# Kernel tuning notes

Hardware: AMD Instinct MI355X
Metric: run time of the kernel (lower is better)

The kernel has to match this reference:

```python
import jax, jax.numpy as jnp
import numpy as np

EMBED = 1024
HEADS = 16
DK = EMBED // HEADS
DFF = 4 * EMBED
EPS = 1e-5


def layer_norm(x, g, b):
    mu = jnp.mean(x, axis=-1, keepdims=True)
    var = jnp.var(x, axis=-1, keepdims=True)
    return (x - mu) * jax.lax.rsqrt(var + EPS) * g + b


def setup_inputs() -> dict:
    key = jax.random.key(0)
    ks = jax.random.split(key, 12)
    s = lambda d: 1.0 / np.sqrt(d)
    return {
        "x": jax.random.normal(ks[0], (4, 1024, EMBED), dtype=jnp.float32),
        "norm_g": jnp.ones((EMBED,), jnp.float32),
        "norm_b": jnp.zeros((EMBED,), jnp.float32),
        "w_qkv": jax.random.normal(ks[1], (EMBED, 3 * EMBED), jnp.float32) * s(EMBED),
        "b_qkv": jnp.zeros((3 * EMBED,), jnp.float32),
        "w_proj": jax.random.normal(ks[2], (EMBED, EMBED), jnp.float32) * s(EMBED),
        "b_proj": jnp.zeros((EMBED,), jnp.float32),
        "w_fc1": jax.random.normal(ks[3], (EMBED, DFF), jnp.float32) * s(EMBED),
        "b_fc1": jnp.zeros((DFF,), jnp.float32),
        "w_fc2": jax.random.normal(ks[4], (DFF, EMBED), jnp.float32) * s(DFF),
        "b_fc2": jnp.zeros((EMBED,), jnp.float32),
    }


def reference(x, norm_g, norm_b, w_qkv, b_qkv, w_proj, b_proj, w_fc1, b_fc1, w_fc2, b_fc2):
    B, N, C = x.shape
    # --- attention branch (pre-norm, shared norm params) ---
    h = layer_norm(x, norm_g, norm_b)
    qkv = (h @ w_qkv + b_qkv).reshape(B, N, 3, HEADS, DK)
    q, k, v = jnp.moveaxis(qkv, 2, 0)  # each [B, N, H, dk]
    # NOTE: source divides by dk**(-0.5), i.e. multiplies scores by sqrt(dk)
    scores = jnp.einsum('bnhd,bmhd->bhnm', q, k) * (DK ** 0.5)
    attn = jax.nn.softmax(scores, axis=-1)
    ctx = jnp.einsum('bhnm,bmhd->bnhd', attn, v).reshape(B, N, C)
    x = x + (ctx @ w_proj + b_proj)
    # --- MLP branch ---
    h = layer_norm(x, norm_g, norm_b)
    h = jax.nn.gelu(h @ w_fc1 + b_fc1, approximate=False)
    x = x + (h @ w_fc2 + b_fc2)
    return x
```

## Files before the change

### kernel.cpp

```cpp
#include <hip/hip_runtime.h>
#include <hip/hip_bf16.h>

typedef __attribute__((ext_vector_type(8))) short short8;
typedef __attribute__((ext_vector_type(8))) _Float16 half8;
typedef __attribute__((ext_vector_type(4))) float f32x4;

__device__ __forceinline__ unsigned short f2h(float f) {
    _Float16 h = (_Float16)f;
    return *reinterpret_cast<unsigned short*>(&h);
}
__device__ __forceinline__ float h2f(unsigned short u) {
    _Float16 h = *reinterpret_cast<_Float16*>(&u);
    return (float)h;
}

__device__ __forceinline__ void gld_lds16(const unsigned short* g, unsigned short* l) {
    __builtin_amdgcn_global_load_lds(
        (const __attribute__((address_space(1))) unsigned int*)g,
        (__attribute__((address_space(3))) unsigned int*)l, 16, 0, 0);
}

__global__ __launch_bounds__(256)
void transpose_all(const float* __restrict__ W0, const float* __restrict__ W1,
                   const float* __restrict__ W2, const float* __restrict__ W3,
                   unsigned short* __restrict__ o0, unsigned short* __restrict__ o1,
                   unsigned short* __restrict__ o2, unsigned short* __restrict__ o3) {
    __shared__ float tile[32][33];
    const int bid = blockIdx.x;
    const float* W; unsigned short* out; int K, N, loc;
    if (bid < 3072)      { W = W0; out = o0; K = 1024; N = 3072; loc = bid; }
    else if (bid < 4096) { W = W1; out = o1; K = 1024; N = 1024; loc = bid - 3072; }
    else if (bid < 8192) { W = W2; out = o2; K = 1024; N = 4096; loc = bid - 4096; }
    else                 { W = W3; out = o3; K = 4096; N = 1024; loc = bid - 8192; }
    const int nx = N >> 5;
    const int n0 = (loc % nx) << 5, k0 = (loc / nx) << 5;
    const int tid = threadIdx.x;
    const int r = tid >> 3, c4 = (tid & 7) << 2;
    float4 v = *reinterpret_cast<const float4*>(W + (size_t)(k0 + r) * N + n0 + c4);
    tile[r][c4 + 0] = v.x; tile[r][c4 + 1] = v.y;
    tile[r][c4 + 2] = v.z; tile[r][c4 + 3] = v.w;
    __syncthreads();
    const int n = n0 + r;
    ushort4 o;
    o.x = f2h(tile[c4 + 0][r]); o.y = f2h(tile[c4 + 1][r]);
    o.z = f2h(tile[c4 + 2][r]); o.w = f2h(tile[c4 + 3][r]);
    *reinterpret_cast<ushort4*>(out + (size_t)n * K + k0 + c4) = o;
}

__global__ __launch_bounds__(256)
void ln_kernel(const float* __restrict__ x, const float* __restrict__ gw,
               const float* __restrict__ bw, unsigned short* __restrict__ out) {
    const int row = blockIdx.x, tid = threadIdx.x;
    const float* xr = x + (size_t)row * 1024;
    float4 v = *reinterpret_cast<const float4*>(xr + tid * 4);
    float s = v.x + v.y + v.z + v.w;
    float sq = v.x * v.x + v.y * v.y + v.z * v.z + v.w * v.w;
    #pragma unroll
    for (int off = 1; off < 64; off <<= 1) {
        s  += __shfl_xor(s, off);
        sq += __shfl_xor(sq, off);
    }
    __shared__ float ps[4], pq[4];
    const int wave = tid >> 6;
    if ((tid & 63) == 0) { ps[wave] = s; pq[wave] = sq; }
    __syncthreads();
    s  = ps[0] + ps[1] + ps[2] + ps[3];
    sq = pq[0] + pq[1] + pq[2] + pq[3];
    const float mu = s * (1.0f / 1024.0f);
    const float var = sq * (1.0f / 1024.0f) - mu * mu;
    const float rs = rsqrtf(var + 1e-5f);
    float4 gv = *reinterpret_cast<const float4*>(gw + tid * 4);
    float4 bv = *reinterpret_cast<const float4*>(bw + tid * 4);
    ushort4 o;
    o.x = f2h((v.x - mu) * rs * gv.x + bv.x);
    o.y = f2h((v.y - mu) * rs * gv.y + bv.y);
    o.z = f2h((v.z - mu) * rs * gv.z + bv.z);
    o.w = f2h((v.w - mu) * rs * gv.w + bv.w);
    *reinterpret_cast<ushort4*>(out + (size_t)row * 1024 + tid * 4) = o;
}

template<int EPI>
__global__ __launch_bounds__(512, 2)
void gemm256(const unsigned short* __restrict__ A, const unsigned short* __restrict__ Bt,
             const float* __restrict__ bias, void* Cout,
             int M, int N, int K, int lda, int ldb, int ldc) {
    __shared__ unsigned short As[2][256 * 64];
    __shared__ unsigned short Bs[2][256 * 64];
    const int tid = threadIdx.x;
    const int wave = tid >> 6, lane = tid & 63;
    const int nwg = gridDim.x;
    const int swz = (blockIdx.x & 7) * (nwg >> 3) + (blockIdx.x >> 3);
    const int nx = N >> 8;
    const int bm = (swz / nx) << 8, bn = (swz % nx) << 8;
    const int wm = wave >> 2, wn = wave & 3;
    const int fr = lane & 15, g8 = (lane >> 4) << 3, fq = (lane >> 4) << 2;
    const int jq = g8 >> 3;
    const int sx = fr & 7;

    const int srow = lane >> 3;
    const int scol = ((lane & 7) ^ srow) << 3;
    const unsigned short* gA = A + (size_t)(bm + wave * 32 + srow) * lda + scol;
    const unsigned short* gB = Bt + (size_t)(bn + wave * 32 + srow) * ldb + scol;
    const int lb = wave * 32 * 64;

    f32x4 acc[8][4];
    #pragma unroll
    for (int m = 0; m < 8; ++m)
        #pragma unroll
        for (int n_ = 0; n_ < 4; ++n_)
            #pragma unroll
            for (int r_ = 0; r_ < 4; ++r_) acc[m][n_][r_] = 0.0f;

    auto stage = [&](int buf, int k0) {
        #pragma unroll
        for (int i = 0; i < 4; ++i) {
            gld_lds16(gA + (size_t)(i * 8) * lda + k0, &As[buf][lb + i * 512]);
            gld_lds16(gB + (size_t)(i * 8) * ldb + k0, &Bs[buf][lb + i * 512]);
        }
    };
    auto compute = [&](int buf) {
        half8 bf0[4], bf1[4];
        #pragma unroll
        for (int n_ = 0; n_ < 4; ++n_) {
            const int bb = (wn * 64 + n_ * 16 + fr) * 64;
            bf0[n_] = *reinterpret_cast<const half8*>(&Bs[buf][bb + ((jq ^ sx) << 3)]);
            bf1[n_] = *reinterpret_cast<const half8*>(&Bs[buf][bb + (((4 + jq) ^ sx) << 3)]);
        }
        #pragma unroll
        for (int m = 0; m < 8; ++m) {
            const int ab = (wm * 128 + m * 16 + fr) * 64;
            half8 a0 = *reinterpret_cast<const half8*>(&As[buf][ab + ((jq ^ sx) << 3)]);
            half8 a1 = *reinterpret_cast<const half8*>(&As[buf][ab + (((4 + jq) ^ sx) << 3)]);
            #pragma unroll
            for (int n_ = 0; n_ < 4; ++n_) {
                acc[m][n_] = __builtin_amdgcn_mfma_f32_16x16x32_f16(a0, bf0[n_], acc[m][n_], 0, 0, 0);
                acc[m][n_] = __builtin_amdgcn_mfma_f32_16x16x32_f16(a1, bf1[n_], acc[m][n_], 0, 0, 0);
            }
        }
    };

    stage(0, 0);
    __syncthreads();
    const int NT = K >> 6;
    for (int t = 0; t < NT; ++t) {
        const int cur = t & 1;
        if (t + 1 < NT) stage(cur ^ 1, (t + 1) << 6);
        compute(cur);
        __syncthreads();
    }

    unsigned short* o16 = reinterpret_cast<unsigned short*>(Cout);
    #pragma unroll
    for (int n_ = 0; n_ < 4; ++n_) {
        const int col = bn + wn * 64 + n_ * 16 + fr;
        const float bc = bias[col];
        #pragma unroll
        for (int m = 0; m < 8; ++m) {
            #pragma unroll
            for (int r_ = 0; r_ < 4; ++r_) {
                const int row = bm + wm * 128 + m * 16 + fq + r_;
                const size_t idx = (size_t)row * ldc + col;
                float v = acc[m][n_][r_] + bc;
                if (EPI == 0) {
                    o16[idx] = f2h(v);
                } else {
                    float ge = 0.5f * v * (1.0f + erff(v * 0.70710678118654752f));
                    o16[idx] = f2h(ge);
                }
            }
        }
    }
}

template<int EPI, int BM>
__global__ __launch_bounds__(256)
void gemm_bt(const unsigned short* __restrict__ A, const unsigned short* __restrict__ Bt,
             const float* __restrict__ bias, const float* resid,
             void* Cout, int M, int N, int K, int lda, int ldb, int ldc) {
    constexpr int MF = BM / 32;
    __shared__ unsigned short As[2][BM * 32];
    __shared__ unsigned short Bs[2][128 * 32];
    const int tid = threadIdx.x;
    const int wave = tid >> 6, lane = tid & 63;
    const int bm = blockIdx.y * BM, bn = blockIdx.x << 7;
    const int wr = (wave >> 1) * (BM / 2), wc = (wave & 1) << 6;
    const int fr = lane & 15, g8 = (lane >> 4) << 3, fq = (lane >> 4) << 2;
    const int jq = g8 >> 3, sx2 = (fr >> 1) & 3;
    const size_t koff = (EPI == 3) ? (size_t)blockIdx.z * K : 0;

    const int srowA = (BM == 128) ? ((wave << 5) + (lane >> 2)) : ((wave << 4) + (lane >> 2));
    const int srowB = (wave << 5) + (lane >> 2);
    const int scol = (((lane & 3) ^ ((lane >> 3) & 3))) << 3;
    const unsigned short* gA0 = A + (size_t)(bm + srowA) * lda + scol + koff;
    const unsigned short* gA1 = gA0 + (size_t)16 * lda;
    const unsigned short* gB0 = Bt + (size_t)(bn + srowB) * ldb + scol + koff;
    const unsigned short* gB1 = gB0 + (size_t)16 * ldb;

    f32x4 acc[MF][4];
    #pragma unroll
    for (int m = 0; m < MF; ++m)
        #pragma unroll
        for (int n = 0; n < 4; ++n)
            #pragma unroll
            for (int r = 0; r < 4; ++r) acc[m][n][r] = 0.0f;

    auto stage = [&](int buf, int k0) {
        unsigned short* lA = &As[buf][(BM == 128) ? (wave << 10) : (wave << 9)];
        unsigned short* lB = &Bs[buf][wave << 10];
        gld_lds16(gA0 + k0, lA);
        if constexpr (BM == 128) gld_lds16(gA1 + k0, lA + 512);
        gld_lds16(gB0 + k0, lB);
        gld_lds16(gB1 + k0, lB + 512);
    };
    auto compute = [&](int buf) {
        half8 af[MF], bfv[4];
        #pragma unroll
        for (int m = 0; m < MF; ++m)
            af[m] = *reinterpret_cast<const half8*>(
                &As[buf][(wr + m * 16 + fr) * 32 + ((jq ^ sx2) << 3)]);
        #pragma unroll
        for (int n = 0; n < 4; ++n)
            bfv[n] = *reinterpret_cast<const half8*>(
                &Bs[buf][(wc + n * 16 + fr) * 32 + ((jq ^ sx2) << 3)]);
        #pragma unroll
        for (int m = 0; m < MF; ++m)
            #pragma unroll
            for (int n = 0; n < 4; ++n)
                acc[m][n] = __builtin_amdgcn_mfma_f32_16x16x32_f16(af[m], bfv[n], acc[m][n], 0, 0, 0);
    };

    const int nt = K >> 5;
    stage(0, 0);
    __syncthreads();
    int k0 = 32;
    for (int t = 0; t < nt - 2; t += 2) {
        stage(1, k0);
        compute(0);
        __syncthreads();
        stage(0, k0 + 32);
        compute(1);
        __syncthreads();
        k0 += 64;
    }
    stage(1, k0);
    compute(0);
    __syncthreads();
    compute(1);

    if (EPI == 3) {
        float* P = reinterpret_cast<float*>(Cout) + (size_t)blockIdx.z * (size_t)M * ldc;
        #pragma unroll
        for (int n = 0; n < 4; ++n) {
            const int col = bn + wc + n * 16 + fr;
            #pragma unroll
            for (int m = 0; m < MF; ++m)
                #pragma unroll
                for (int r = 0; r < 4; ++r) {
                    const int row = bm + wr + m * 16 + fq + r;
                    P[(size_t)row * ldc + col] = acc[m][n][r];
                }
        }
        return;
    }

    #pragma unroll
    for (int n = 0; n < 4; ++n) {
        const int col = bn + wc + n * 16 + fr;
        const float bc = bias[col];
        #pragma unroll
        for (int m = 0; m < MF; ++m) {
            #pragma unroll
            for (int r = 0; r < 4; ++r) {
                const int row = bm + wr + m * 16 + fq + r;
                const size_t idx = (size_t)row * ldc + col;
                float v = acc[m][n][r] + bc;
                reinterpret_cast<float*>(Cout)[idx] = v + resid[idx];
            }
        }
    }
}

template<int Z>
__global__ __launch_bounds__(256)
void red_kernel(const float* __restrict__ p, const float* __restrict__ bias,
                float* out) {
    const size_t MN = (size_t)4096 * 1024;
    const size_t i = ((size_t)blockIdx.x * 256 + threadIdx.x) * 4;
    float4 r  = *reinterpret_cast<const float4*>(out + i);
    float4 bb = *reinterpret_cast<const float4*>(bias + (i & 1023));
    float o0 = r.x + bb.x, o1 = r.y + bb.y, o2 = r.z + bb.z, o3 = r.w + bb.w;
    #pragma unroll
    for (int z = 0; z < Z; ++z) {
        float4 a = *reinterpret_cast<const float4*>(p + (size_t)z * MN + i);
        o0 += a.x; o1 += a.y; o2 += a.z; o3 += a.w;
    }
    float4 o; o.x = o0; o.y = o1; o.z = o2; o.w = o3;
    *reinterpret_cast<float4*>(out + i) = o;
}

__global__ __launch_bounds__(256)
void kv_conv(const unsigned short* __restrict__ qkv16, unsigned short* __restrict__ K_g,
             unsigned short* __restrict__ Vt_g) {
    __shared__ unsigned short VtT[64][72];
    const int kc = blockIdx.x;
    const int bh = blockIdx.y;
    const int b = bh >> 4, h = bh & 15;
    const int tid = threadIdx.x;
    const int key = tid >> 2, c16 = (tid & 3) << 4;
    const unsigned short* kp = qkv16 + ((size_t)(b * 1024 + kc * 64 + key)) * 3072 + 1024 + h * 64 + c16;
    alignas(16) unsigned short kbuf[16];
    #pragma unroll
    for (int j = 0; j < 16; j += 8) {
        short8 k8 = *reinterpret_cast<const short8*>(kp + j);
        short8 v8 = *reinterpret_cast<const short8*>(kp + 1024 + j);
        #pragma unroll
        for (int c = 0; c < 8; ++c) {
            kbuf[j + c] = f2h(8.0f * h2f((unsigned short)k8[c]));
            VtT[c16 + j + c][key] = (unsigned short)v8[c];
        }
    }
    const size_t kb = ((size_t)bh * 1024 + kc * 64 + key) * 64 + c16;
    *reinterpret_cast<short8*>(K_g + kb)     = *reinterpret_cast<short8*>(&kbuf[0]);
    *reinterpret_cast<short8*>(K_g + kb + 8) = *reinterpret_cast<short8*>(&kbuf[8]);
    __syncthreads();
    const int d = tid >> 2;
    const size_t vb = ((size_t)bh * 64 + d) * 1024 + (size_t)kc * 64 + c16;
    *reinterpret_cast<short8*>(Vt_g + vb)     = *reinterpret_cast<const short8*>(&VtT[d][c16]);
    *reinterpret_cast<short8*>(Vt_g + vb + 8) = *reinterpret_cast<const short8*>(&VtT[d][c16 + 8]);
}

__global__ __launch_bounds__(256)
void attn_kernel(const unsigned short* __restrict__ qkv16,
                 const unsigned short* __restrict__ K_g,
                 const unsigned short* __restrict__ Vt_g,
                 unsigned short* __restrict__ ctx) {
    __shared__ unsigned short Kh[64][72];
    __shared__ unsigned short Vt[64][72];
    __shared__ unsigned short Plds[4][16][72];
    const int qt = blockIdx.x;
    const int bh = blockIdx.y;
    const int b = bh >> 4, h = bh & 15;
    const int tid = threadIdx.x;
    const int wave = tid >> 6, lane = tid & 63;
    const int fr = lane & 15, g8 = (lane >> 4) << 3, fq = (lane >> 4) << 2;

    const int qrow = qt * 64 + wave * 16 + fr;
    const unsigned short* qp = qkv16 + ((size_t)(b * 1024 + qrow)) * 3072 + h * 64;
    half8 qf[2];
    qf[0] = *reinterpret_cast<const half8*>(qp + g8);
    qf[1] = *reinterpret_cast<const half8*>(qp + 32 + g8);

    float mrun[4], lrun[4];
    f32x4 cacc[4];
    #pragma unroll
    for (int r = 0; r < 4; ++r) { mrun[r] = -3.0e38f; lrun[r] = 0.0f; }
    #pragma unroll
    for (int nd = 0; nd < 4; ++nd)
        #pragma unroll
        for (int r = 0; r < 4; ++r) cacc[nd][r] = 0.0f;

    const int skey = tid >> 2, sc16 = (tid & 3) << 4;
    const unsigned short* kgp = K_g + ((size_t)bh * 1024 + skey) * 64 + sc16;
    const unsigned short* vgp = Vt_g + ((size_t)bh * 64 + skey) * 1024 + sc16;

    short8 ka = *reinterpret_cast<const short8*>(kgp);
    short8 kb = *reinterpret_cast<const short8*>(kgp + 8);
    short8 va = *reinterpret_cast<const short8*>(vgp);
    short8 vb = *reinterpret_cast<const short8*>(vgp + 8);

    for (int kt = 0; kt < 16; ++kt) {
        __syncthreads();
        *reinterpret_cast<short8*>(&Kh[skey][sc16])     = ka;
        *reinterpret_cast<short8*>(&Kh[skey][sc16 + 8]) = kb;
        *reinterpret_cast<short8*>(&Vt[skey][sc16])     = va;
        *reinterpret_cast<short8*>(&Vt[skey][sc16 + 8]) = vb;
        __syncthreads();
        const int ktn = (kt < 15) ? kt + 1 : 15;
        ka = *reinterpret_cast<const short8*>(kgp + (size_t)ktn * 4096);
        kb = *reinterpret_cast<const short8*>(kgp + (size_t)ktn * 4096 + 8);
        va = *reinterpret_cast<const short8*>(vgp + ktn * 64);
        vb = *reinterpret_cast<const short8*>(vgp + ktn * 64 + 8);

        f32x4 S[4];
        #pragma unroll
        for (int n = 0; n < 4; ++n)
            #pragma unroll
            for (int r = 0; r < 4; ++r) S[n][r] = 0.0f;
        #pragma unroll
        for (int s_ = 0; s_ < 2; ++s_)
            #pragma unroll
            for (int n = 0; n < 4; ++n) {
                half8 kh = *reinterpret_cast<const half8*>(&Kh[n * 16 + fr][s_ * 32 + g8]);
                S[n] = __builtin_amdgcn_mfma_f32_16x16x32_f16(qf[s_], kh, S[n], 0, 0, 0);
            }

        float mt[4];
        #pragma unroll
        for (int r = 0; r < 4; ++r)
            mt[r] = fmaxf(fmaxf(S[0][r], S[1][r]), fmaxf(S[2][r], S[3][r]));
        #pragma unroll
        for (int r = 0; r < 4; ++r) {
            mt[r] = fmaxf(mt[r], __shfl_xor(mt[r], 1));
            mt[r] = fmaxf(mt[r], __shfl_xor(mt[r], 2));
            mt[r] = fmaxf(mt[r], __shfl_xor(mt[r], 4));
            mt[r] = fmaxf(mt[r], __shfl_xor(mt[r], 8));
        }
        float P[4][4], rsum[4];
        #pragma unroll
        for (int r = 0; r < 4; ++r) {
            float mnew = fmaxf(mrun[r], mt[r]);
            float sf = __expf(mrun[r] - mnew);
            mrun[r] = mnew;
            rsum[r] = 0.0f;
            #pragma unroll
            for (int n = 0; n < 4; ++n) {
                float p = __expf(S[n][r] - mnew);
                P[n][r] = p;
                rsum[r] += p;
            }
            lrun[r] *= sf;
            #pragma unroll
            for (int nd = 0; nd < 4; ++nd) cacc[nd][r] *= sf;
        }
        #pragma unroll
        for (int r = 0; r < 4; ++r) {
            rsum[r] += __shfl_xor(rsum[r], 1);
            rsum[r] += __shfl_xor(rsum[r], 2);
            rsum[r] += __shfl_xor(rsum[r], 4);
            rsum[r] += __shfl_xor(rsum[r], 8);
            lrun[r] += rsum[r];
        }
        #pragma unroll
        for (int n = 0; n < 4; ++n)
            #pragma unroll
            for (int r = 0; r < 4; ++r)
                Plds[wave][fq + r][n * 16 + fr] = f2h(P[n][r]);
        #pragma unroll
        for (int s_ = 0; s_ < 2; ++s_) {
            half8 pa = *reinterpret_cast<const half8*>(&Plds[wave][fr][s_ * 32 + g8]);
            #pragma unroll
            for (int nd = 0; nd < 4; ++nd) {
                half8 vb8 = *reinterpret_cast<const half8*>(&Vt[nd * 16 + fr][s_ * 32 + g8]);
                cacc[nd] = __builtin_amdgcn_mfma_f32_16x16x32_f16(pa, vb8, cacc[nd], 0, 0, 0);
            }
        }
    }
    #pragma unroll
    for (int r = 0; r < 4; ++r) {
        const float inv = 1.0f / lrun[r];
        const int row = qt * 64 + wave * 16 + fq + r;
        unsigned short* cp = ctx + ((size_t)(b * 1024 + row)) * 1024 + h * 64;
        #pragma unroll
        for (int nd = 0; nd < 4; ++nd)
            cp[nd * 16 + fr] = f2h(cacc[nd][r] * inv);
    }
}

extern "C" void kernel_launch(void* const* d_in, const int* in_sizes, int n_in,
                              void* d_out, int out_size, void* d_ws, size_t ws_size,
                              hipStream_t stream) {
    const float* x      = (const float*)d_in[0];
    const float* norm_g = (const float*)d_in[1];
    const float* norm_b = (const float*)d_in[2];
    const float* w_qkv  = (const float*)d_in[3];
    const float* b_qkv  = (const float*)d_in[4];
    const float* w_proj = (const float*)d_in[5];
    const float* b_proj = (const float*)d_in[6];
    const float* w_fc1  = (const float*)d_in[7];
    const float* b_fc1  = (const float*)d_in[8];
    const float* w_fc2  = (const float*)d_in[9];
    const float* b_fc2  = (const float*)d_in[10];
    float* out = (float*)d_out;
    char* ws = (char*)d_ws;

    size_t off = 0;
    unsigned short* wqkvT  = (unsigned short*)(ws + off); off += (size_t)3072 * 1024 * 2;
    unsigned short* wprojT = (unsigned short*)(ws + off); off += (size_t)1024 * 1024 * 2;
    unsigned short* wfc1T  = (unsigned short*)(ws + off); off += (size_t)4096 * 1024 * 2;
    unsigned short* wfc2T  = (unsigned short*)(ws + off); off += (size_t)1024 * 4096 * 2;
    unsigned short* ctxb   = (unsigned short*)(ws + off); off += (size_t)4096 * 1024 * 2;
    char* G = ws + off;
    unsigned short* h1    = (unsigned short*)G;
    unsigned short* qkv16 = (unsigned short*)(G + (size_t)8388608);
    unsigned short* K_g   = (unsigned short*)G;
    unsigned short* Vt_g  = (unsigned short*)(G + (size_t)33554432);
    unsigned short* fc1o  = (unsigned short*)G;
    unsigned short* h2    = (unsigned short*)(G + (size_t)41943040);
    float*          fc2p  = (float*)(G + (size_t)50331648);

    transpose_all<<<12288, 256, 0, stream>>>(w_qkv, w_proj, w_fc1, w_fc2,
                                             wqkvT, wprojT, wfc1T, wfc2T);

    ln_kernel<<<4096, 256, 0, stream>>>(x, norm_g, norm_b, h1);
    gemm256<0><<<192, 512, 0, stream>>>(h1, wqkvT, b_qkv, qkv16,
                                        4096, 3072, 1024, 1024, 1024, 3072);

    kv_conv<<<dim3(16, 64), 256, 0, stream>>>(qkv16, K_g, Vt_g);

    attn_kernel<<<dim3(16, 64), 256, 0, stream>>>(qkv16, K_g, Vt_g, ctxb);

    gemm_bt<1, 64><<<dim3(8, 64), 256, 0, stream>>>(ctxb, wprojT, b_proj, x, out,
                                                    4096, 1024, 1024, 1024, 1024, 1024);

    ln_kernel<<<4096, 256, 0, stream>>>(out, norm_g, norm_b, h2);
    gemm256<2><<<256, 512, 0, stream>>>(h2, wfc1T, b_fc1, fc1o,
                                        4096, 4096, 1024, 1024, 1024, 4096);

    gemm_bt<3, 64><<<dim3(8, 64, 2), 256, 0, stream>>>(fc1o, wfc2T, nullptr, nullptr, fc2p,
                                                       4096, 1024, 2048, 4096, 4096, 1024);
    red_kernel<2><<<4096, 256, 0, stream>>>(fc2p, b_fc2, out);
}
```

Before: 275.6 us.

## Shrink gemm256 tile to 128x256 with triple-buffered LDS pipeline

Halves the M dimension of the big GEMM tile from 256 to 128 and doubles the grid, so the QKV and FC1 GEMMs launch more workgroups and fill the 256 CUs better. It also replaces the double-buffered loop, which synchronised twice per step, with a three-stage ring: loads run two tiles ahead, and one waitcnt plus barrier guards each step. The accumulators drop from 8x4 to 4x4 fragments, which eases register pressure. The cost is less reuse per tile and more redundant B-tile traffic, and the hand-placed vmcnt counts must match exactly the six loads each thread issues per stage.

```diff
diff --git a/kernel.cpp b/kernel.cpp
--- a/kernel.cpp
+++ b/kernel.cpp
@@ -84,14 +84,14 @@
 void gemm256(const unsigned short* __restrict__ A, const unsigned short* __restrict__ Bt,
              const float* __restrict__ bias, void* Cout,
              int M, int N, int K, int lda, int ldb, int ldc) {
-    __shared__ unsigned short As[2][256 * 64];
-    __shared__ unsigned short Bs[2][256 * 64];
+    __shared__ unsigned short As[3][128 * 64];
+    __shared__ unsigned short Bs[3][256 * 64];
     const int tid = threadIdx.x;
     const int wave = tid >> 6, lane = tid & 63;
     const int nwg = gridDim.x;
     const int swz = (blockIdx.x & 7) * (nwg >> 3) + (blockIdx.x >> 3);
     const int nx = N >> 8;
-    const int bm = (swz / nx) << 8, bn = (swz % nx) << 8;
+    const int bm = (swz / nx) << 7, bn = (swz % nx) << 8;
     const int wm = wave >> 2, wn = wave & 3;
     const int fr = lane & 15, g8 = (lane >> 4) << 3, fq = (lane >> 4) << 2;
     const int jq = g8 >> 3;
@@ -99,55 +99,68 @@
 
     const int srow = lane >> 3;
     const int scol = ((lane & 7) ^ srow) << 3;
-    const unsigned short* gA = A + (size_t)(bm + wave * 32 + srow) * lda + scol;
+    const unsigned short* gA = A + (size_t)(bm + wave * 16 + srow) * lda + scol;
     const unsigned short* gB = Bt + (size_t)(bn + wave * 32 + srow) * ldb + scol;
-    const int lb = wave * 32 * 64;
-
-    f32x4 acc[8][4];
-    #pragma unroll
-    for (int m = 0; m < 8; ++m)
+    const int lbA = wave * 16 * 64;
+    const int lbB = wave * 32 * 64;
+
+    f32x4 acc[4][4];
+    #pragma unroll
+    for (int m = 0; m < 4; ++m)
         #pragma unroll
         for (int n_ = 0; n_ < 4; ++n_)
             #pragma unroll
             for (int r_ = 0; r_ < 4; ++r_) acc[m][n_][r_] = 0.0f;
 
     auto stage = [&](int buf, int k0) {
-        #pragma unroll
-        for (int i = 0; i < 4; ++i) {
-            gld_lds16(gA + (size_t)(i * 8) * lda + k0, &As[buf][lb + i * 512]);
-            gld_lds16(gB + (size_t)(i * 8) * ldb + k0, &Bs[buf][lb + i * 512]);
-        }
+        gld_lds16(gA + k0, &As[buf][lbA]);
+        gld_lds16(gA + (size_t)8 * lda + k0, &As[buf][lbA + 512]);
+        #pragma unroll
+        for (int i = 0; i < 4; ++i)
+            gld_lds16(gB + (size_t)(i * 8) * ldb + k0, &Bs[buf][lbB + i * 512]);
     };
     auto compute = [&](int buf) {
-        half8 bf0[4], bf1[4];
+        half8 av[4][2], bv[4][2];
         #pragma unroll
         for (int n_ = 0; n_ < 4; ++n_) {
-            const int bb = (wn * 64 + n_ * 16 + fr) * 64;
-            bf0[n_] = *reinterpret_cast<const half8*>(&Bs[buf][bb + ((jq ^ sx) << 3)]);
-            bf1[n_] = *reinterpret_cast<const half8*>(&Bs[buf][bb + (((4 + jq) ^ sx) << 3)]);
-        }
-        #pragma unroll
-        for (int m = 0; m < 8; ++m) {
-            const int ab = (wm * 128 + m * 16 + fr) * 64;
-            half8 a0 = *reinterpret_cast<const half8*>(&As[buf][ab + ((jq ^ sx) << 3)]);
-            half8 a1 = *reinterpret_cast<const half8*>(&As[buf][ab + (((4 + jq) ^ sx) << 3)]);
-            #pragma unroll
-            for (int n_ = 0; n_ < 4; ++n_) {
-                acc[m][n_] = __builtin_amdgcn_mfma_f32_16x16x32_f16(a0, bf0[n_], acc[m][n_], 0, 0, 0);
-                acc[m][n_] = __builtin_amdgcn_mfma_f32_16x16x32_f16(a1, bf1[n_], acc[m][n_], 0, 0, 0);
-            }
-        }
+            const int rb = (wn * 64 + n_ * 16 + fr) * 64;
+            #pragma unroll
+            for (int kk = 0; kk < 2; ++kk)
+                bv[n_][kk] = *reinterpret_cast<const half8*>(
+                    &Bs[buf][rb + (((kk * 4 + jq) ^ sx) << 3)]);
+        }
+        #pragma unroll
+        for (int m = 0; m < 4; ++m) {
+            const int rb = (wm * 64 + m * 16 + fr) * 64;
+            #pragma unroll
+            for (int kk = 0; kk < 2; ++kk)
+                av[m][kk] = *reinterpret_cast<const half8*>(
+                    &As[buf][rb + (((kk * 4 + jq) ^ sx) << 3)]);
+        }
+        #pragma unroll
+        for (int kk = 0; kk < 2; ++kk)
+            #pragma unroll
+            for (int m = 0; m < 4; ++m)
+                #pragma unroll
+                for (int n_ = 0; n_ < 4; ++n_)
+                    acc[m][n_] = __builtin_amdgcn_mfma_f32_16x16x32_f16(
+                        av[m][kk], bv[n_][kk], acc[m][n_], 0, 0, 0);
     };
 
+    const int NT = K >> 6;
     stage(0, 0);
-    __syncthreads();
-    const int NT = K >> 6;
-    for (int t = 0; t < NT; ++t) {
-        const int cur = t & 1;
-        if (t + 1 < NT) stage(cur ^ 1, (t + 1) << 6);
-        compute(cur);
-        __syncthreads();
-    }
+    stage(1, 64);
+    for (int t = 0; t < NT - 1; ++t) {
+        asm volatile("s_waitcnt vmcnt(6)" ::: "memory");
+        __builtin_amdgcn_s_barrier();
+        __builtin_amdgcn_sched_barrier(0);
+        if (t + 2 < NT) stage((t + 2) % 3, (t + 2) << 6);
+        compute(t % 3);
+    }
+    asm volatile("s_waitcnt vmcnt(0)" ::: "memory");
+    __builtin_amdgcn_s_barrier();
+    __builtin_amdgcn_sched_barrier(0);
+    compute((NT - 1) % 3);
 
     unsigned short* o16 = reinterpret_cast<unsigned short*>(Cout);
     #pragma unroll
@@ -155,10 +168,10 @@
         const int col = bn + wn * 64 + n_ * 16 + fr;
         const float bc = bias[col];
         #pragma unroll
-        for (int m = 0; m < 8; ++m) {
+        for (int m = 0; m < 4; ++m) {
             #pragma unroll
             for (int r_ = 0; r_ < 4; ++r_) {
-                const int row = bm + wm * 128 + m * 16 + fq + r_;
+                const int row = bm + wm * 64 + m * 16 + fq + r_;
                 const size_t idx = (size_t)row * ldc + col;
                 float v = acc[m][n_][r_] + bc;
                 if (EPI == 0) {
@@ -492,7 +505,7 @@
                                              wqkvT, wprojT, wfc1T, wfc2T);
 
     ln_kernel<<<4096, 256, 0, stream>>>(x, norm_g, norm_b, h1);
-    gemm256<0><<<192, 512, 0, stream>>>(h1, wqkvT, b_qkv, qkv16,
+    gemm256<0><<<384, 512, 0, stream>>>(h1, wqkvT, b_qkv, qkv16,
                                         4096, 3072, 1024, 1024, 1024, 3072);
 
     kv_conv<<<dim3(16, 64), 256, 0, stream>>>(qkv16, K_g, Vt_g);
@@ -503,7 +516,7 @@
                                                     4096, 1024, 1024, 1024, 1024, 1024);
 
     ln_kernel<<<4096, 256, 0, stream>>>(out, norm_g, norm_b, h2);
-    gemm256<2><<<256, 512, 0, stream>>>(h2, wfc1T, b_fc1, fc1o,
+    gemm256<2><<<512, 512, 0, stream>>>(h2, wfc1T, b_fc1, fc1o,
                                         4096, 4096, 1024, 1024, 1024, 4096);
 
     gemm_bt<3, 64><<<dim3(8, 64, 2), 256, 0, stream>>>(fc1o, wfc2T, nullptr, nullptr, fc2p,
```

New measurement: 305.1 us. +10.7%, slower.

## Shrink QKV/FC1 GEMM tiles and split FC2 four ways with fp16 partials

Applied to the files above, without the earlier changes.

Replaces the 256x256x64 GEMM used for QKV and FC1 with a 128x256x32 tile kernel that declares higher occupancy and launches twice as many blocks. The goal is better CU fill, since 192 or 256 large blocks do not fill the GPU. FC2 split-K goes from 2 to 4 slices and stores partials as fp16 instead of fp32, which cuts partial-buffer traffic. The cost is less data reuse per tile, an fp16 rounding error on each partial sum, and a reduction kernel that reads four slices.

```diff
diff --git a/kernel.cpp b/kernel.cpp
--- a/kernel.cpp
+++ b/kernel.cpp
@@ -80,74 +80,78 @@
 }
 
 template<int EPI>
-__global__ __launch_bounds__(512, 2)
-void gemm256(const unsigned short* __restrict__ A, const unsigned short* __restrict__ Bt,
-             const float* __restrict__ bias, void* Cout,
-             int M, int N, int K, int lda, int ldb, int ldc) {
-    __shared__ unsigned short As[2][256 * 64];
-    __shared__ unsigned short Bs[2][256 * 64];
+__global__ __launch_bounds__(512, 4)
+void gemm_mid(const unsigned short* __restrict__ A, const unsigned short* __restrict__ Bt,
+              const float* __restrict__ bias, void* Cout,
+              int M, int N, int K, int lda, int ldb, int ldc) {
+    __shared__ unsigned short As[2][128 * 32];
+    __shared__ unsigned short Bs[2][256 * 32];
     const int tid = threadIdx.x;
     const int wave = tid >> 6, lane = tid & 63;
     const int nwg = gridDim.x;
     const int swz = (blockIdx.x & 7) * (nwg >> 3) + (blockIdx.x >> 3);
     const int nx = N >> 8;
-    const int bm = (swz / nx) << 8, bn = (swz % nx) << 8;
+    const int bm = (swz / nx) << 7, bn = (swz % nx) << 8;
     const int wm = wave >> 2, wn = wave & 3;
     const int fr = lane & 15, g8 = (lane >> 4) << 3, fq = (lane >> 4) << 2;
     const int jq = g8 >> 3;
-    const int sx = fr & 7;
-
-    const int srow = lane >> 3;
-    const int scol = ((lane & 7) ^ srow) << 3;
-    const unsigned short* gA = A + (size_t)(bm + wave * 32 + srow) * lda + scol;
-    const unsigned short* gB = Bt + (size_t)(bn + wave * 32 + srow) * ldb + scol;
-    const int lb = wave * 32 * 64;
-
-    f32x4 acc[8][4];
-    #pragma unroll
-    for (int m = 0; m < 8; ++m)
+    const int sx2 = (fr >> 1) & 3;
+
+    const int srow = lane >> 2;
+    const int scol = ((lane & 3) ^ ((lane >> 3) & 3)) << 3;
+    const unsigned short* gA  = A + (size_t)(bm + wave * 16 + srow) * lda + scol;
+    const unsigned short* gB0 = Bt + (size_t)(bn + wave * 32 + srow) * ldb + scol;
+    const unsigned short* gB1 = gB0 + (size_t)16 * ldb;
+    const int lbA = wave * 512;
+    const int lbB = wave * 1024;
+
+    f32x4 acc[4][4];
+    #pragma unroll
+    for (int m = 0; m < 4; ++m)
         #pragma unroll
         for (int n_ = 0; n_ < 4; ++n_)
             #pragma unroll
             for (int r_ = 0; r_ < 4; ++r_) acc[m][n_][r_] = 0.0f;
 
     auto stage = [&](int buf, int k0) {
-        #pragma unroll
-        for (int i = 0; i < 4; ++i) {
-            gld_lds16(gA + (size_t)(i * 8) * lda + k0, &As[buf][lb + i * 512]);
-            gld_lds16(gB + (size_t)(i * 8) * ldb + k0, &Bs[buf][lb + i * 512]);
-        }
+        gld_lds16(gA + k0, &As[buf][lbA]);
+        gld_lds16(gB0 + k0, &Bs[buf][lbB]);
+        gld_lds16(gB1 + k0, &Bs[buf][lbB + 512]);
     };
     auto compute = [&](int buf) {
-        half8 bf0[4], bf1[4];
-        #pragma unroll
-        for (int n_ = 0; n_ < 4; ++n_) {
-            const int bb = (wn * 64 + n_ * 16 + fr) * 64;
-            bf0[n_] = *reinterpret_cast<const half8*>(&Bs[buf][bb + ((jq ^ sx) << 3)]);
-            bf1[n_] = *reinterpret_cast<const half8*>(&Bs[buf][bb + (((4 + jq) ^ sx) << 3)]);
-        }
-        #pragma unroll
-        for (int m = 0; m < 8; ++m) {
-            const int ab = (wm * 128 + m * 16 + fr) * 64;
-            half8 a0 = *reinterpret_cast<const half8*>(&As[buf][ab + ((jq ^ sx) << 3)]);
-            half8 a1 = *reinterpret_cast<const half8*>(&As[buf][ab + (((4 + jq) ^ sx) << 3)]);
-            #pragma unroll
-            for (int n_ = 0; n_ < 4; ++n_) {
-                acc[m][n_] = __builtin_amdgcn_mfma_f32_16x16x32_f16(a0, bf0[n_], acc[m][n_], 0, 0, 0);
-                acc[m][n_] = __builtin_amdgcn_mfma_f32_16x16x32_f16(a1, bf1[n_], acc[m][n_], 0, 0, 0);
-            }
-        }
+        half8 af[4], bfv[4];
+        #pragma unroll
+        for (int m = 0; m < 4; ++m)
+            af[m] = *reinterpret_cast<const half8*>(
+                &As[buf][(wm * 64 + m * 16 + fr) * 32 + ((jq ^ sx2) << 3)]);
+        #pragma unroll
+        for (int n_ = 0; n_ < 4; ++n_)
+            bfv[n_] = *reinterpret_cast<const half8*>(
+                &Bs[buf][(wn * 64 + n_ * 16 + fr) * 32 + ((jq ^ sx2) << 3)]);
+        #pragma unroll
+        for (int m = 0; m < 4; ++m)
+            #pragma unroll
+            for (int n_ = 0; n_ < 4; ++n_)
+                acc[m][n_] = __builtin_amdgcn_mfma_f32_16x16x32_f16(af[m], bfv[n_], acc[m][n_], 0, 0, 0);
     };
 
+    const int nt = K >> 5;
     stage(0, 0);
     __syncthreads();
-    const int NT = K >> 6;
-    for (int t = 0; t < NT; ++t) {
-        const int cur = t & 1;
-        if (t + 1 < NT) stage(cur ^ 1, (t + 1) << 6);
-        compute(cur);
+    int k0 = 32;
+    for (int t = 0; t < nt - 2; t += 2) {
+        stage(1, k0);
+        compute(0);
         __syncthreads();
-    }
+        stage(0, k0 + 32);
+        compute(1);
+        __syncthreads();
+        k0 += 64;
+    }
+    stage(1, k0);
+    compute(0);
+    __syncthreads();
+    compute(1);
 
     unsigned short* o16 = reinterpret_cast<unsigned short*>(Cout);
     #pragma unroll
@@ -155,10 +159,10 @@
         const int col = bn + wn * 64 + n_ * 16 + fr;
         const float bc = bias[col];
         #pragma unroll
-        for (int m = 0; m < 8; ++m) {
+        for (int m = 0; m < 4; ++m) {
             #pragma unroll
             for (int r_ = 0; r_ < 4; ++r_) {
-                const int row = bm + wm * 128 + m * 16 + fq + r_;
+                const int row = bm + wm * 64 + m * 16 + fq + r_;
                 const size_t idx = (size_t)row * ldc + col;
                 float v = acc[m][n_][r_] + bc;
                 if (EPI == 0) {
@@ -186,7 +190,7 @@
     const int wr = (wave >> 1) * (BM / 2), wc = (wave & 1) << 6;
     const int fr = lane & 15, g8 = (lane >> 4) << 3, fq = (lane >> 4) << 2;
     const int jq = g8 >> 3, sx2 = (fr >> 1) & 3;
-    const size_t koff = (EPI == 3) ? (size_t)blockIdx.z * K : 0;
+    const size_t koff = (EPI >= 3) ? (size_t)blockIdx.z * K : 0;
 
     const int srowA = (BM == 128) ? ((wave << 5) + (lane >> 2)) : ((wave << 4) + (lane >> 2));
     const int srowB = (wave << 5) + (lane >> 2);
@@ -247,8 +251,9 @@
     __syncthreads();
     compute(1);
 
-    if (EPI == 3) {
-        float* P = reinterpret_cast<float*>(Cout) + (size_t)blockIdx.z * (size_t)M * ldc;
+    if (EPI == 4) {
+        unsigned short* P = reinterpret_cast<unsigned short*>(Cout) +
+                            (size_t)blockIdx.z * (size_t)M * ldc;
         #pragma unroll
         for (int n = 0; n < 4; ++n) {
             const int col = bn + wc + n * 16 + fr;
@@ -257,7 +262,7 @@
                 #pragma unroll
                 for (int r = 0; r < 4; ++r) {
                     const int row = bm + wr + m * 16 + fq + r;
-                    P[(size_t)row * ldc + col] = acc[m][n][r];
+                    P[(size_t)row * ldc + col] = f2h(acc[m][n][r]);
                 }
         }
         return;
@@ -282,8 +287,8 @@
 
 template<int Z>
 __global__ __launch_bounds__(256)
-void red_kernel(const float* __restrict__ p, const float* __restrict__ bias,
-                float* out) {
+void red_h(const unsigned short* __restrict__ p, const float* __restrict__ bias,
+           float* out) {
     const size_t MN = (size_t)4096 * 1024;
     const size_t i = ((size_t)blockIdx.x * 256 + threadIdx.x) * 4;
     float4 r  = *reinterpret_cast<const float4*>(out + i);
@@ -291,8 +296,8 @@
     float o0 = r.x + bb.x, o1 = r.y + bb.y, o2 = r.z + bb.z, o3 = r.w + bb.w;
     #pragma unroll
     for (int z = 0; z < Z; ++z) {
-        float4 a = *reinterpret_cast<const float4*>(p + (size_t)z * MN + i);
-        o0 += a.x; o1 += a.y; o2 += a.z; o3 += a.w;
+        ushort4 a = *reinterpret_cast<const ushort4*>(p + (size_t)z * MN + i);
+        o0 += h2f(a.x); o1 += h2f(a.y); o2 += h2f(a.z); o3 += h2f(a.w);
     }
     float4 o; o.x = o0; o.y = o1; o.z = o2; o.w = o3;
     *reinterpret_cast<float4*>(out + i) = o;
@@ -486,14 +491,14 @@
     unsigned short* Vt_g  = (unsigned short*)(G + (size_t)33554432);
     unsigned short* fc1o  = (unsigned short*)G;
     unsigned short* h2    = (unsigned short*)(G + (size_t)41943040);
-    float*          fc2p  = (float*)(G + (size_t)50331648);
+    unsigned short* fc2ph = (unsigned short*)(G + (size_t)33554432);
 
     transpose_all<<<12288, 256, 0, stream>>>(w_qkv, w_proj, w_fc1, w_fc2,
                                              wqkvT, wprojT, wfc1T, wfc2T);
 
     ln_kernel<<<4096, 256, 0, stream>>>(x, norm_g, norm_b, h1);
-    gemm256<0><<<192, 512, 0, stream>>>(h1, wqkvT, b_qkv, qkv16,
-                                        4096, 3072, 1024, 1024, 1024, 3072);
+    gemm_mid<0><<<384, 512, 0, stream>>>(h1, wqkvT, b_qkv, qkv16,
+                                         4096, 3072, 1024, 1024, 1024, 3072);
 
     kv_conv<<<dim3(16, 64), 256, 0, stream>>>(qkv16, K_g, Vt_g);
 
@@ -503,10 +508,10 @@
                                                     4096, 1024, 1024, 1024, 1024, 1024);
 
     ln_kernel<<<4096, 256, 0, stream>>>(out, norm_g, norm_b, h2);
-    gemm256<2><<<256, 512, 0, stream>>>(h2, wfc1T, b_fc1, fc1o,
-                                        4096, 4096, 1024, 1024, 1024, 4096);
-
-    gemm_bt<3, 64><<<dim3(8, 64, 2), 256, 0, stream>>>(fc1o, wfc2T, nullptr, nullptr, fc2p,
-                                                       4096, 1024, 2048, 4096, 4096, 1024);
-    red_kernel<2><<<4096, 256, 0, stream>>>(fc2p, b_fc2, out);
-}
+    gemm_mid<2><<<512, 512, 0, stream>>>(h2, wfc1T, b_fc1, fc1o,
+                                         4096, 4096, 1024, 1024, 1024, 4096);
+
+    gemm_bt<4, 64><<<dim3(8, 64, 4), 256, 0, stream>>>(fc1o, wfc2T, nullptr, nullptr, fc2ph,
+                                                       4096, 1024, 1024, 4096, 4096, 1024);
+    red_h<4><<<4096, 256, 0, stream>>>(fc2ph, b_fc2, out);
+}
```

Result: slower. 284.1 us (+3.1%).
